# Optimization experiments

Measured on AMD Instinct MI355X. Metric: run time of the kernel, lower is better.

## Reference

```python
import jax, jax.numpy as jnp
import numpy as np

T = 2048          # tokens
H = 32            # query heads
HKV = 4           # kv heads
D = 128           # head dim
HID = 2048        # hidden size
EPS = 1e-6
THETA = 10000.0


def _rmsnorm(x, w):
    # x: [..., D]
    var = jnp.mean(x * x, axis=-1, keepdims=True)
    return x * jax.lax.rsqrt(var + EPS) * w


def _rope(x, positions):
    # neox-style rotary: x [T, h, D], positions [T]
    half = D // 2
    inv_freq = 1.0 / (THETA ** (jnp.arange(half, dtype=jnp.float32) * 2.0 / D))
    freqs = positions.astype(jnp.float32)[:, None] * inv_freq        # [T, D/2]
    cos = jnp.cos(freqs)[:, None, :]                                  # [T, 1, D/2]
    sin = jnp.sin(freqs)[:, None, :]
    x1, x2 = x[..., :half], x[..., half:]
    return jnp.concatenate([x1 * cos - x2 * sin, x2 * cos + x1 * sin], axis=-1)


def setup_inputs() -> dict:
    key = jax.random.key(0)
    k1, k2, k3 = jax.random.split(key, 3)
    scale_in = 1.0 / np.sqrt(HID)
    scale_o = 1.0 / np.sqrt(H * D)
    return {
        "hidden_states": jax.random.normal(k1, (T, HID), dtype=jnp.float32),
        "positions": jnp.arange(T, dtype=jnp.int32),
        "w_qkv": jax.random.normal(k2, (HID, (H + 2 * HKV) * D), dtype=jnp.float32) * scale_in,
        "w_o": jax.random.normal(k3, (H * D, HID), dtype=jnp.float32) * scale_o,
        "q_norm_w": jnp.ones((D,), dtype=jnp.float32),
        "k_norm_w": jnp.ones((D,), dtype=jnp.float32),
    }


def reference(hidden_states, positions, w_qkv, w_o, q_norm_w, k_norm_w):
    q_size, kv_size = H * D, HKV * D
    qkv = hidden_states @ w_qkv                                       # [T, (H+2*HKV)*D]
    q = qkv[:, :q_size].reshape(T, H, D)
    k = qkv[:, q_size:q_size + kv_size].reshape(T, HKV, D)
    v = qkv[:, q_size + kv_size:].reshape(T, HKV, D)

    # per-head RMSNorm on q/k, then RoPE
    q = _rope(_rmsnorm(q, q_norm_w), positions)
    k = _rope(_rmsnorm(k, k_norm_w), positions)

    # GQA: expand kv heads to query heads
    rep = H // HKV
    k = jnp.repeat(k, rep, axis=1)                                    # [T, H, D]
    v = jnp.repeat(v, rep, axis=1)

    scaling = D ** -0.5
    scores = jnp.einsum('qhd,khd->hqk', q, k) * scaling               # [H, T, T]
    causal = jnp.tril(jnp.ones((T, T), dtype=bool))
    scores = jnp.where(causal[None], scores, jnp.finfo(scores.dtype).min)
    probs = jax.nn.softmax(scores, axis=-1)
    attn = jnp.einsum('hqk,khd->qhd', probs, v).reshape(T, H * D)
    return attn @ w_o                                                 # [T, HID]
```

## Files before the change

kernel.cpp:

```cpp
#include <hip/hip_runtime.h>
#include <hip/hip_bf16.h>

typedef __attribute__((ext_vector_type(8))) __bf16 bf16x8;
typedef __attribute__((ext_vector_type(4))) __bf16 bf16x4;
typedef __attribute__((ext_vector_type(4))) float f32x4;
typedef __attribute__((ext_vector_type(16))) float f32x16;

#define T_TOK 2048
#define NH 32
#define NKV 4
#define HD 128
#define HID 2048
#define QKV_N 5120
#define QSZ 4096
#define KOFF 4096
#define VOFF 4608
#define ATT_N 4096

#define GLOAD_LDS16(g, l)                                              \
  __builtin_amdgcn_global_load_lds(                                    \
      (const __attribute__((address_space(1))) void*)(g),              \
      (__attribute__((address_space(3))) void*)(l), 16, 0, 0)

__global__ __launch_bounds__(256) void cast_f32_bf16(const float* __restrict__ in,
                                                     __bf16* __restrict__ out, int n4) {
  int i = blockIdx.x * 256 + threadIdx.x;
  if (i < n4) {
    float4 v = reinterpret_cast<const float4*>(in)[i];
    bf16x4 o;
    o[0] = (__bf16)v.x; o[1] = (__bf16)v.y; o[2] = (__bf16)v.z; o[3] = (__bf16)v.w;
    reinterpret_cast<bf16x4*>(out)[i] = o;
  }
}

__global__ __launch_bounds__(256) void transpose_cast(const float* __restrict__ in,
                                                      __bf16* __restrict__ out,
                                                      int R, int C) {
  __shared__ __attribute__((aligned(16))) __bf16 tile[64][72];
  const int c0 = blockIdx.x * 64;
  const int r0 = blockIdx.y * 64;
  const int ca = (threadIdx.x & 15) * 4;
  const int ra = (threadIdx.x >> 4) * 4;
  float4 v[4];
#pragma unroll
  for (int i = 0; i < 4; ++i)
    v[i] = *reinterpret_cast<const float4*>(&in[(size_t)(r0 + ra + i) * C + c0 + ca]);
#pragma unroll
  for (int j = 0; j < 4; ++j) {
    bf16x4 o;
#pragma unroll
    for (int i = 0; i < 4; ++i) o[i] = (__bf16)(((const float*)&v[i])[j]);
    *reinterpret_cast<bf16x4*>(&tile[ca + j][ra]) = o;
  }
  __syncthreads();
#pragma unroll
  for (int i = 0; i < 2; ++i) {
    int c = i * 32 + (threadIdx.x >> 3);
    int r8 = (threadIdx.x & 7) * 8;
    bf16x8 o = *reinterpret_cast<const bf16x8*>(&tile[c][r8]);
    *reinterpret_cast<bf16x8*>(&out[(size_t)(c0 + c) * R + r0 + r8]) = o;
  }
}

__global__ __launch_bounds__(256) void v_transpose(const __bf16* __restrict__ qkv,
                                                   __bf16* __restrict__ vt) {
  __shared__ __bf16 tile[64][72];
  int t0 = blockIdx.x * 64;
  int d0 = blockIdx.y * 64;
  int kvh = blockIdx.z;
  int tx = threadIdx.x & 63;
  int ty = threadIdx.x >> 6;
#pragma unroll
  for (int i = 0; i < 64; i += 4)
    tile[ty + i][tx] = qkv[(size_t)(t0 + ty + i) * QKV_N + VOFF + kvh * HD + d0 + tx];
  __syncthreads();
#pragma unroll
  for (int i = 0; i < 64; i += 4)
    vt[((size_t)kvh * HD + d0 + ty + i) * T_TOK + t0 + tx] = tile[tx][ty + i];
}

template <int OUTF32>
__global__ __launch_bounds__(256) void gemm_v9(const __bf16* __restrict__ A,
                                               const __bf16* __restrict__ B,
                                               void* __restrict__ Cp,
                                               int M, int N, int Ktot, int KS,
                                               int nby, int nks) {
  __shared__ __attribute__((aligned(16))) __bf16 As[3][128][32];
  __shared__ __attribute__((aligned(16))) __bf16 Bs[3][128][32];
  const int tid = threadIdx.x;
  const int lane = tid & 63;
  const int wave = tid >> 6;
  const int la = lane & 15;
  const int lb = lane >> 4;
  const int wr = (wave >> 1) * 64;
  const int wc = (wave & 1) * 64;

  const int nwg = gridDim.x;
  const int cpx = nwg >> 3;
  const int swz = ((int)blockIdx.x & 7) * cpx + ((int)blockIdx.x >> 3);
  const int ks = swz % nks;
  const int t2 = swz / nks;
  const int by = t2 % nby;
  const int bx = t2 / nby;
  const int rowA0 = by * 128;
  const int rowB0 = bx * 128;
  const int k00 = ks * KS;

  const int srow = wave * 16 + (lane >> 2);
  const int scol = (((lane & 3) * 16) ^ (((lane >> 2) & 3) << 4)) >> 1;
  const __bf16* Asrc0 = &A[(size_t)(rowA0 + srow) * Ktot + k00 + scol];
  const __bf16* Asrc1 = &A[(size_t)(rowA0 + 64 + srow) * Ktot + k00 + scol];
  const __bf16* Bsrc0 = &B[(size_t)(rowB0 + srow) * Ktot + k00 + scol];
  const __bf16* Bsrc1 = &B[(size_t)(rowB0 + 64 + srow) * Ktot + k00 + scol];

#define STAGEG(b, k0)                                            \
  do {                                                           \
    GLOAD_LDS16(Asrc0 + (k0), &As[b][wave * 16][0]);             \
    GLOAD_LDS16(Asrc1 + (k0), &As[b][64 + wave * 16][0]);        \
    GLOAD_LDS16(Bsrc0 + (k0), &Bs[b][wave * 16][0]);             \
    GLOAD_LDS16(Bsrc1 + (k0), &Bs[b][64 + wave * 16][0]);        \
  } while (0)

  f32x4 acc[4][4] = {};

  const int nt = KS >> 5;
  STAGEG(0, 0);
  STAGEG(1, 32);
  asm volatile("s_waitcnt vmcnt(4)" ::: "memory");
  __builtin_amdgcn_s_barrier();
  __builtin_amdgcn_sched_barrier(0);

  const int rdswz = (lb * 16) ^ ((la & 3) << 4);

  int cur = 0, stg = 2;
  for (int t = 0; t < nt; ++t) {
    if (t + 2 < nt) {
      STAGEG(stg, (t + 2) * 32);
    }

    const char* Ab = (const char*)&As[cur][0][0];
    const char* Bb = (const char*)&Bs[cur][0][0];
    bf16x8 af[4], bfr[4];
#pragma unroll
    for (int m = 0; m < 4; ++m)
      af[m] = *reinterpret_cast<const bf16x8*>(Ab + (wr + m * 16 + la) * 64 + rdswz);
#pragma unroll
    for (int n = 0; n < 4; ++n)
      bfr[n] = *reinterpret_cast<const bf16x8*>(Bb + (wc + n * 16 + la) * 64 + rdswz);
    __builtin_amdgcn_s_setprio(1);
#pragma unroll
    for (int m = 0; m < 4; ++m)
#pragma unroll
      for (int n = 0; n < 4; ++n)
        acc[m][n] = __builtin_amdgcn_mfma_f32_16x16x32_bf16(af[m], bfr[n], acc[m][n], 0, 0, 0);
    __builtin_amdgcn_s_setprio(0);

    const int rem = nt - 1 - t;
    if (rem >= 2) {
      asm volatile("s_waitcnt vmcnt(4)" ::: "memory");
    } else if (rem == 1) {
      asm volatile("s_waitcnt vmcnt(0)" ::: "memory");
    }
    if (rem) {
      __builtin_amdgcn_sched_barrier(0);
      __builtin_amdgcn_s_barrier();
      __builtin_amdgcn_sched_barrier(0);
    }
    cur = (cur == 2) ? 0 : cur + 1;
    stg = (stg == 2) ? 0 : stg + 1;
  }
#undef STAGEG

#pragma unroll
  for (int m = 0; m < 4; ++m) {
#pragma unroll
    for (int n = 0; n < 4; ++n) {
#pragma unroll
      for (int r = 0; r < 4; ++r) {
        int row = rowA0 + wr + m * 16 + lb * 4 + r;
        int col = rowB0 + wc + n * 16 + la;
        if (OUTF32) {
          float* pp = (float*)Cp + (size_t)ks * M * N;
          pp[(size_t)row * N + col] = acc[m][n][r];
        } else {
          reinterpret_cast<__bf16*>(Cp)[(size_t)row * N + col] = (__bf16)acc[m][n][r];
        }
      }
    }
  }
}

__global__ __launch_bounds__(256) void reduce2_f32(const float* __restrict__ pp,
                                                   float* __restrict__ out, int n4) {
  int i = blockIdx.x * 256 + threadIdx.x;
  if (i < n4) {
    float4 a = reinterpret_cast<const float4*>(pp)[i];
    float4 b = reinterpret_cast<const float4*>(pp + (size_t)HID * T_TOK)[i];
    float4 o;
    o.x = a.x + b.x; o.y = a.y + b.y; o.z = a.z + b.z; o.w = a.w + b.w;
    reinterpret_cast<float4*>(out)[i] = o;
  }
}

__global__ __launch_bounds__(64) void rope_table(const int* __restrict__ positions,
                                                 float* __restrict__ tab) {
  const int t = blockIdx.x;
  const int d = threadIdx.x;
  float freq = exp2f(-(float)d * 0.20762050593046015f);
  float fr = (float)positions[t] * freq;
  float c, s;
  sincosf(fr, &s, &c);
  tab[t * 128 + d] = c;
  tab[t * 128 + 64 + d] = s;
}

__global__ __launch_bounds__(128) void norm_rope(__bf16* __restrict__ qkv,
                                                 const float* __restrict__ tab,
                                                 const float* __restrict__ qw,
                                                 const float* __restrict__ kw) {
  const int t = blockIdx.x;
  const int head = blockIdx.y;
  const bool is_q = head < NH;
  const int col = is_q ? head * HD : KOFF + (head - NH) * HD;
  __bf16* row = qkv + (size_t)t * QKV_N + col;
  const int d = threadIdx.x;
  float x = (float)row[d];
  float ss = x * x;
#pragma unroll
  for (int mm = 1; mm < 64; mm <<= 1) ss += __shfl_xor(ss, mm);
  __shared__ float red[2];
  __shared__ float yl[128];
  if ((d & 63) == 0) red[d >> 6] = ss;
  __syncthreads();
  float var = (red[0] + red[1]) * (1.0f / 128.0f);
  float sc = rsqrtf(var + 1e-6f);
  const float* wv = is_q ? qw : kw;
  yl[d] = x * sc * wv[d];
  __syncthreads();
  if (d < 64) {
    float x1 = yl[d], x2 = yl[d + 64];
    float c = tab[t * 128 + d];
    float sn = tab[t * 128 + 64 + d];
    row[d] = (__bf16)(x1 * c - x2 * sn);
    row[d + 64] = (__bf16)(x2 * c + x1 * sn);
  }
}

__device__ __forceinline__ uint32_t pkbf(float a, float b) {
  union { __bf16 h; unsigned short u; } x, y;
  x.h = (__bf16)a;
  y.h = (__bf16)b;
  return (uint32_t)x.u | ((uint32_t)y.u << 16);
}

__global__ __launch_bounds__(256, 2) void flash_attn5(const __bf16* __restrict__ qkv,
                                                      const __bf16* __restrict__ vt,
                                                      __bf16* __restrict__ attn) {
  __shared__ __attribute__((aligned(16))) __bf16 lds[32768];

  const int tid = threadIdx.x;
  const int lane = tid & 63;
  const int wave = tid >> 6;
  const int q5 = lane & 31;
  const int hi = lane >> 5;
  const int yy = blockIdx.x;
  const int kvh = yy >> 1;
  const int h = kvh * 8 + (yy & 1) * 4 + wave;
  const __bf16* Kbase = qkv + KOFF + kvh * HD;
  const __bf16* Vbase = vt + (size_t)kvh * HD * T_TOK;

  const int qt = 63 - (int)blockIdx.y;
  const int qb = qt * 32;
  const int qrow = qb + q5;
  const int nt = (qb + 32 + 63) >> 6;

  const float qscale = 0.088388347648318447f * 1.4426950408889634f;

  bf16x8 qf[8];
  {
    const __bf16* Qp = qkv + (size_t)(qb + q5) * QKV_N + h * HD + hi * 8;
#pragma unroll
    for (int k0 = 0; k0 < 8; ++k0) {
      bf16x8 q = *reinterpret_cast<const bf16x8*>(Qp + k0 * 16);
#pragma unroll
      for (int j = 0; j < 8; ++j) q[j] = (__bf16)((float)q[j] * qscale);
      qf[k0] = q;
    }
  }

  const int kc = (lane & 15) * 16;
  const int vc = (lane & 7) * 16;

#define STAGE5(b, kv00)                                                         \
  do {                                                                          \
    __bf16* kdst = lds + (b) * 8192;                                            \
    __bf16* vdst = lds + 16384 + (b) * 8192;                                    \
    _Pragma("unroll")                                                           \
    for (int i = 0; i < 4; ++i) {                                               \
      int kr = wave * 16 + i * 4 + (lane >> 4);                                 \
      int ksc = (kc ^ ((kr & 15) << 4)) >> 1;                                   \
      GLOAD_LDS16(Kbase + (size_t)((kv00) + kr) * QKV_N + ksc,                  \
                  kdst + (wave * 16 + i * 4) * 128);                            \
      int vr = wave * 32 + i * 8 + (lane >> 3);                                 \
      int vsc = (vc ^ ((vr & 7) << 4)) >> 1;                                    \
      GLOAD_LDS16(Vbase + (size_t)vr * T_TOK + (kv00) + vsc,                    \
                  vdst + (wave * 32 + i * 8) * 64);                             \
    }                                                                           \
  } while (0)

  f32x16 acc0 = {}, acc1 = {}, acc2 = {}, acc3 = {};
  float mrow = -1e30f, lrow = 0.0f;

  STAGE5(0, 0);

  int cur = 0;
  for (int t = 0; t < nt; ++t) {
    const int kv0 = t * 64;
    __builtin_amdgcn_s_barrier();
    __builtin_amdgcn_sched_barrier(0);
    if (t + 1 < nt) {
      STAGE5(cur ^ 1, kv0 + 64);
      asm volatile("s_waitcnt vmcnt(8)" ::: "memory");
    } else {
      asm volatile("s_waitcnt vmcnt(0)" ::: "memory");
    }
    __builtin_amdgcn_s_barrier();
    __builtin_amdgcn_sched_barrier(0);

    const char* Kt = (const char*)(lds + cur * 8192);
    const char* Vt = (const char*)(lds + 16384 + cur * 8192);

    f32x16 st0 = {}, st1 = {};
    __builtin_amdgcn_s_setprio(1);
#pragma unroll
    for (int k0 = 0; k0 < 8; ++k0) {
      int cS = (k0 * 32 + hi * 16) ^ ((q5 & 15) << 4);
      bf16x8 a0 = *reinterpret_cast<const bf16x8*>(Kt + q5 * 256 + cS);
      bf16x8 a1 = *reinterpret_cast<const bf16x8*>(Kt + (32 + q5) * 256 + cS);
      st0 = __builtin_amdgcn_mfma_f32_32x32x16_bf16(a0, qf[k0], st0, 0, 0, 0);
      st1 = __builtin_amdgcn_mfma_f32_32x32x16_bf16(a1, qf[k0], st1, 0, 0, 0);
    }
    __builtin_amdgcn_s_setprio(0);

    if (!(kv0 + 63 <= qb)) {
#pragma unroll
      for (int r = 0; r < 16; ++r) {
        int kp = kv0 + (r & 3) + 8 * (r >> 2) + 4 * hi;
        if (kp > qrow) st0[r] = -1e30f;
        if (kp + 32 > qrow) st1[r] = -1e30f;
      }
    }
    float mx = -1e30f;
#pragma unroll
    for (int r = 0; r < 16; ++r) mx = fmaxf(mx, fmaxf(st0[r], st1[r]));
    mx = fmaxf(mx, __shfl_xor(mx, 32));
    if (__any(mx > mrow + 8.0f)) {
      float mnew = fmaxf(mrow, mx);
      float corr = exp2f(mrow - mnew);
      lrow *= corr;
      acc0 *= corr; acc1 *= corr; acc2 *= corr; acc3 *= corr;
      mrow = mnew;
    }
    float ps = 0.0f;
#pragma unroll
    for (int r = 0; r < 16; ++r) {
      float p0 = exp2f(st0[r] - mrow);
      float p1 = exp2f(st1[r] - mrow);
      ps += p0 + p1;
      st0[r] = p0;
      st1[r] = p1;
    }
    ps += __shfl_xor(ps, 32);
    lrow += ps;

    uint32_t W0[8], W1[8];
#pragma unroll
    for (int m = 0; m < 8; ++m) {
      W0[m] = pkbf(st0[2 * m], st0[2 * m + 1]);
      W1[m] = pkbf(st1[2 * m], st1[2 * m + 1]);
    }

    const bool hib = (hi != 0);
#pragma unroll
    for (int ks = 0; ks < 4; ++ks) {
      const int j = 4 * (ks & 1);
      uint32_t wj0, wj1, wj2, wj3;
      if (ks < 2) { wj0 = W0[j]; wj1 = W0[j + 1]; wj2 = W0[j + 2]; wj3 = W0[j + 3]; }
      else        { wj0 = W1[j]; wj1 = W1[j + 1]; wj2 = W1[j + 2]; wj3 = W1[j + 3]; }
      uint32_t keepA = hib ? wj2 : wj0;
      uint32_t keepB = hib ? wj3 : wj1;
      uint32_t sendA = hib ? wj0 : wj2;
      uint32_t sendB = hib ? wj1 : wj3;
      uint32_t recvA = (uint32_t)__shfl_xor((int)sendA, 32);
      uint32_t recvB = (uint32_t)__shfl_xor((int)sendB, 32);
      union { uint32_t u[4]; bf16x8 v; } fr;
      fr.u[0] = hib ? recvA : keepA;
      fr.u[1] = hib ? recvB : keepB;
      fr.u[2] = hib ? keepA : recvA;
      fr.u[3] = hib ? keepB : recvB;
      const int cV = (ks * 32 + hi * 16) ^ ((q5 & 7) << 4);
      __builtin_amdgcn_s_setprio(1);
      bf16x8 v0 = *reinterpret_cast<const bf16x8*>(Vt + (0 * 32 + q5) * 128 + cV);
      acc0 = __builtin_amdgcn_mfma_f32_32x32x16_bf16(v0, fr.v, acc0, 0, 0, 0);
      bf16x8 v1 = *reinterpret_cast<const bf16x8*>(Vt + (1 * 32 + q5) * 128 + cV);
      acc1 = __builtin_amdgcn_mfma_f32_32x32x16_bf16(v1, fr.v, acc1, 0, 0, 0);
      bf16x8 v2 = *reinterpret_cast<const bf16x8*>(Vt + (2 * 32 + q5) * 128 + cV);
      acc2 = __builtin_amdgcn_mfma_f32_32x32x16_bf16(v2, fr.v, acc2, 0, 0, 0);
      bf16x8 v3 = *reinterpret_cast<const bf16x8*>(Vt + (3 * 32 + q5) * 128 + cV);
      acc3 = __builtin_amdgcn_mfma_f32_32x32x16_bf16(v3, fr.v, acc3, 0, 0, 0);
      __builtin_amdgcn_s_setprio(0);
    }
    cur ^= 1;
  }

  __syncthreads();
  {
    char* ob = (char*)lds + wave * 8192;
    float inv = 1.0f / lrow;
    const int swzE = (q5 & 15) << 4;
#pragma unroll
    for (int dt = 0; dt < 4; ++dt) {
      f32x16 a = dt == 0 ? acc0 : dt == 1 ? acc1 : dt == 2 ? acc2 : acc3;
#pragma unroll
      for (int t4 = 0; t4 < 4; ++t4) {
        uint2 wv;
        wv.x = pkbf(a[4 * t4] * inv, a[4 * t4 + 1] * inv);
        wv.y = pkbf(a[4 * t4 + 2] * inv, a[4 * t4 + 3] * inv);
        int d2 = (dt * 32 + 8 * t4 + 4 * hi) * 2;
        *reinterpret_cast<uint2*>(ob + q5 * 256 + (d2 ^ swzE)) = wv;
      }
    }
#pragma unroll
    for (int rr = 0; rr < 8; ++rr) {
      int idx = rr * 64 + lane;
      int q = idx >> 4;
      int cc = (idx & 15) * 16;
      bf16x8 o = *reinterpret_cast<const bf16x8*>(ob + q * 256 + (cc ^ ((q & 15) << 4)));
      *reinterpret_cast<bf16x8*>(&attn[(size_t)(qb + q) * ATT_N + h * HD + (cc >> 1)]) = o;
    }
  }
}

extern "C" void kernel_launch(void* const* d_in, const int* in_sizes, int n_in,
                              void* d_out, int out_size, void* d_ws, size_t ws_size,
                              hipStream_t stream) {
  const float* hs   = (const float*)d_in[0];
  const int*   pos  = (const int*)d_in[1];
  const float* wqkv = (const float*)d_in[2];
  const float* wo   = (const float*)d_in[3];
  const float* qw   = (const float*)d_in[4];
  const float* kw   = (const float*)d_in[5];
  float* out = (float*)d_out;

  char* p = (char*)d_ws;
  __bf16* hsb   = (__bf16*)p; p += (size_t)T_TOK * HID * 2;
  __bf16* wqkvT = (__bf16*)p; p += (size_t)QKV_N * HID * 2;
  __bf16* woT   = (__bf16*)p; p += (size_t)HID * QSZ * 2;
  __bf16* qkvb  = (__bf16*)p; p += (size_t)T_TOK * QKV_N * 2;
  __bf16* attnb = (__bf16*)p; p += (size_t)T_TOK * QSZ * 2;
  __bf16* vtb   = (__bf16*)p; p += (size_t)NKV * HD * T_TOK * 2;
  float*  ropet = (float*)p;  p += (size_t)T_TOK * HD * 4;
  float*  oprt  = (float*)p;  p += (size_t)2 * T_TOK * HID * 4;

  cast_f32_bf16<<<(T_TOK * HID / 4) / 256, 256, 0, stream>>>(hs, hsb, T_TOK * HID / 4);
  transpose_cast<<<dim3(QKV_N / 64, HID / 64), 256, 0, stream>>>(wqkv, wqkvT, HID, QKV_N);
  transpose_cast<<<dim3(HID / 64, QSZ / 64), 256, 0, stream>>>(wo, woT, QSZ, HID);
  rope_table<<<T_TOK, 64, 0, stream>>>(pos, ropet);
  gemm_v9<0><<<(QKV_N / 128) * (T_TOK / 128), 256, 0, stream>>>(
      hsb, wqkvT, qkvb, T_TOK, QKV_N, HID, HID, T_TOK / 128, 1);
  norm_rope<<<dim3(T_TOK, NH + NKV), 128, 0, stream>>>(qkvb, ropet, qw, kw);
  v_transpose<<<dim3(T_TOK / 64, HD / 64, NKV), 256, 0, stream>>>(qkvb, vtb);
  flash_attn5<<<dim3(8, 64), 256, 0, stream>>>(qkvb, vtb, attnb);
  gemm_v9<1><<<2 * (HID / 128) * (T_TOK / 128), 256, 0, stream>>>(
      attnb, woT, oprt, T_TOK, HID, QSZ, QSZ / 2, T_TOK / 128, 2);
  reduce2_f32<<<(T_TOK * HID / 4 + 255) / 256, 256, 0, stream>>>(
      oprt, out, T_TOK * HID / 4);
}
```

Measured before the change: 250.3 us.

## Split attention KV range across two wave groups with in-block softmax merge

The flash attention kernel now launches 512 threads per block. Two groups of four waves each process half of the KV tiles for the same query tile, using 32-key tiles instead of 64. At the end, the second group writes its partial outputs (stored as bf16) and its row max and sum to LDS, and the first group merges them with rescaling before the store. This aims to raise occupancy and parallelism and shorten the serial KV loop, at the cost of 64KB of LDS per block, extra barriers, a merge pass, and bf16 rounding of the partial accumulators.

```diff
diff --git a/kernel.cpp b/kernel.cpp
--- a/kernel.cpp
+++ b/kernel.cpp
@@ -253,26 +253,32 @@
   return (uint32_t)x.u | ((uint32_t)y.u << 16);
 }
 
-__global__ __launch_bounds__(256, 2) void flash_attn5(const __bf16* __restrict__ qkv,
+__global__ __launch_bounds__(512, 4) void flash_attn6(const __bf16* __restrict__ qkv,
                                                       const __bf16* __restrict__ vt,
                                                       __bf16* __restrict__ attn) {
-  __shared__ __attribute__((aligned(16))) __bf16 lds[32768];
+  __shared__ __attribute__((aligned(16))) char ldsB[65536];
 
   const int tid = threadIdx.x;
   const int lane = tid & 63;
   const int wave = tid >> 6;
+  const int half = wave >> 2;
+  const int wh = wave & 3;
   const int q5 = lane & 31;
   const int hi = lane >> 5;
-  const int yy = blockIdx.x;
-  const int kvh = yy >> 1;
-  const int h = kvh * 8 + (yy & 1) * 4 + wave;
+  const int xx = blockIdx.x;
+  const int kvh = xx >> 1;
+  const int h = kvh * 8 + (xx & 1) * 4 + wh;
   const __bf16* Kbase = qkv + KOFF + kvh * HD;
   const __bf16* Vbase = vt + (size_t)kvh * HD * T_TOK;
 
   const int qt = 63 - (int)blockIdx.y;
   const int qb = qt * 32;
   const int qrow = qb + q5;
-  const int nt = (qb + 32 + 63) >> 6;
+  const int nt = qt + 1;
+  const int mid = nt >> 1;
+  const int iters = nt - mid;
+  const int tbase = half ? mid : 0;
+  const int mycnt = half ? iters : mid;
 
   const float qscale = 0.088388347648318447f * 1.4426950408889634f;
 
@@ -288,144 +294,176 @@
     }
   }
 
-  const int kc = (lane & 15) * 16;
-  const int vc = (lane & 7) * 16;
-
-#define STAGE5(b, kv00)                                                         \
-  do {                                                                          \
-    __bf16* kdst = lds + (b) * 8192;                                            \
-    __bf16* vdst = lds + 16384 + (b) * 8192;                                    \
-    _Pragma("unroll")                                                           \
-    for (int i = 0; i < 4; ++i) {                                               \
-      int kr = wave * 16 + i * 4 + (lane >> 4);                                 \
-      int ksc = (kc ^ ((kr & 15) << 4)) >> 1;                                   \
-      GLOAD_LDS16(Kbase + (size_t)((kv00) + kr) * QKV_N + ksc,                  \
-                  kdst + (wave * 16 + i * 4) * 128);                            \
-      int vr = wave * 32 + i * 8 + (lane >> 3);                                 \
-      int vsc = (vc ^ ((vr & 7) << 4)) >> 1;                                    \
-      GLOAD_LDS16(Vbase + (size_t)vr * T_TOK + (kv00) + vsc,                    \
-                  vdst + (wave * 32 + i * 8) * 64);                             \
-    }                                                                           \
+  const int ku0 = wh * 2, ku1 = wh * 2 + 1;
+  const int krow0 = ku0 * 4 + (lane >> 4);
+  const int krow1 = ku1 * 4 + (lane >> 4);
+  const int kcB = (lane & 15) * 16;
+  const int ksc0 = (kcB ^ ((krow0 & 15) << 4)) >> 1;
+  const int ksc1 = (kcB ^ ((krow1 & 15) << 4)) >> 1;
+  const int vrow0 = ku0 * 16 + (lane >> 2);
+  const int vrow1 = ku1 * 16 + (lane >> 2);
+  const int vcB = (lane & 3) * 16;
+  const int vsc0 = (vcB ^ ((vrow0 & 3) << 4)) >> 1;
+  const int vsc1 = (vcB ^ ((vrow1 & 3) << 4)) >> 1;
+
+#define STAGE6(b, kv00)                                                        \
+  do {                                                                         \
+    char* base = ldsB + ((b) * 2 + half) * 16384;                              \
+    GLOAD_LDS16(Kbase + (size_t)((kv00) + krow0) * QKV_N + ksc0,               \
+                base + ku0 * 1024);                                            \
+    GLOAD_LDS16(Kbase + (size_t)((kv00) + krow1) * QKV_N + ksc1,               \
+                base + ku1 * 1024);                                            \
+    GLOAD_LDS16(Vbase + (size_t)vrow0 * T_TOK + (kv00) + vsc0,                 \
+                base + 8192 + ku0 * 1024);                                     \
+    GLOAD_LDS16(Vbase + (size_t)vrow1 * T_TOK + (kv00) + vsc1,                 \
+                base + 8192 + ku1 * 1024);                                     \
   } while (0)
 
   f32x16 acc0 = {}, acc1 = {}, acc2 = {}, acc3 = {};
   float mrow = -1e30f, lrow = 0.0f;
 
-  STAGE5(0, 0);
+  if (mycnt > 0) STAGE6(0, tbase * 32);
 
   int cur = 0;
-  for (int t = 0; t < nt; ++t) {
-    const int kv0 = t * 64;
+  for (int t = 0; t < iters; ++t) {
     __builtin_amdgcn_s_barrier();
     __builtin_amdgcn_sched_barrier(0);
-    if (t + 1 < nt) {
-      STAGE5(cur ^ 1, kv0 + 64);
-      asm volatile("s_waitcnt vmcnt(8)" ::: "memory");
+    if (t + 1 < mycnt) {
+      STAGE6(cur ^ 1, (tbase + t + 1) * 32);
+      asm volatile("s_waitcnt vmcnt(4)" ::: "memory");
     } else {
       asm volatile("s_waitcnt vmcnt(0)" ::: "memory");
     }
     __builtin_amdgcn_s_barrier();
     __builtin_amdgcn_sched_barrier(0);
 
-    const char* Kt = (const char*)(lds + cur * 8192);
-    const char* Vt = (const char*)(lds + 16384 + cur * 8192);
-
-    f32x16 st0 = {}, st1 = {};
-    __builtin_amdgcn_s_setprio(1);
-#pragma unroll
-    for (int k0 = 0; k0 < 8; ++k0) {
-      int cS = (k0 * 32 + hi * 16) ^ ((q5 & 15) << 4);
-      bf16x8 a0 = *reinterpret_cast<const bf16x8*>(Kt + q5 * 256 + cS);
-      bf16x8 a1 = *reinterpret_cast<const bf16x8*>(Kt + (32 + q5) * 256 + cS);
-      st0 = __builtin_amdgcn_mfma_f32_32x32x16_bf16(a0, qf[k0], st0, 0, 0, 0);
-      st1 = __builtin_amdgcn_mfma_f32_32x32x16_bf16(a1, qf[k0], st1, 0, 0, 0);
-    }
-    __builtin_amdgcn_s_setprio(0);
-
-    if (!(kv0 + 63 <= qb)) {
+    if (t < mycnt) {
+      const int kv0 = (tbase + t) * 32;
+      const char* Kt = ldsB + (cur * 2 + half) * 16384;
+      const char* Vt = Kt + 8192;
+
+      f32x16 st = {};
+      __builtin_amdgcn_s_setprio(1);
+#pragma unroll
+      for (int k0 = 0; k0 < 8; ++k0) {
+        int cS = (k0 * 32 + hi * 16) ^ ((q5 & 15) << 4);
+        bf16x8 a0 = *reinterpret_cast<const bf16x8*>(Kt + q5 * 256 + cS);
+        st = __builtin_amdgcn_mfma_f32_32x32x16_bf16(a0, qf[k0], st, 0, 0, 0);
+      }
+      __builtin_amdgcn_s_setprio(0);
+
+      if (kv0 + 31 > qb) {
+#pragma unroll
+        for (int r = 0; r < 16; ++r) {
+          int kp = kv0 + (r & 3) + 8 * (r >> 2) + 4 * hi;
+          if (kp > qrow) st[r] = -1e30f;
+        }
+      }
+      float mx = -1e30f;
+#pragma unroll
+      for (int r = 0; r < 16; ++r) mx = fmaxf(mx, st[r]);
+      mx = fmaxf(mx, __shfl_xor(mx, 32));
+      if (__any(mx > mrow + 8.0f)) {
+        float mnew = fmaxf(mrow, mx);
+        float corr = exp2f(mrow - mnew);
+        lrow *= corr;
+        acc0 *= corr; acc1 *= corr; acc2 *= corr; acc3 *= corr;
+        mrow = mnew;
+      }
+      float ps = 0.0f;
 #pragma unroll
       for (int r = 0; r < 16; ++r) {
-        int kp = kv0 + (r & 3) + 8 * (r >> 2) + 4 * hi;
-        if (kp > qrow) st0[r] = -1e30f;
-        if (kp + 32 > qrow) st1[r] = -1e30f;
-      }
-    }
-    float mx = -1e30f;
-#pragma unroll
-    for (int r = 0; r < 16; ++r) mx = fmaxf(mx, fmaxf(st0[r], st1[r]));
-    mx = fmaxf(mx, __shfl_xor(mx, 32));
-    if (__any(mx > mrow + 8.0f)) {
-      float mnew = fmaxf(mrow, mx);
-      float corr = exp2f(mrow - mnew);
-      lrow *= corr;
-      acc0 *= corr; acc1 *= corr; acc2 *= corr; acc3 *= corr;
-      mrow = mnew;
-    }
-    float ps = 0.0f;
-#pragma unroll
-    for (int r = 0; r < 16; ++r) {
-      float p0 = exp2f(st0[r] - mrow);
-      float p1 = exp2f(st1[r] - mrow);
-      ps += p0 + p1;
-      st0[r] = p0;
-      st1[r] = p1;
-    }
-    ps += __shfl_xor(ps, 32);
-    lrow += ps;
-
-    uint32_t W0[8], W1[8];
-#pragma unroll
-    for (int m = 0; m < 8; ++m) {
-      W0[m] = pkbf(st0[2 * m], st0[2 * m + 1]);
-      W1[m] = pkbf(st1[2 * m], st1[2 * m + 1]);
-    }
-
-    const bool hib = (hi != 0);
-#pragma unroll
-    for (int ks = 0; ks < 4; ++ks) {
-      const int j = 4 * (ks & 1);
-      uint32_t wj0, wj1, wj2, wj3;
-      if (ks < 2) { wj0 = W0[j]; wj1 = W0[j + 1]; wj2 = W0[j + 2]; wj3 = W0[j + 3]; }
-      else        { wj0 = W1[j]; wj1 = W1[j + 1]; wj2 = W1[j + 2]; wj3 = W1[j + 3]; }
-      uint32_t keepA = hib ? wj2 : wj0;
-      uint32_t keepB = hib ? wj3 : wj1;
-      uint32_t sendA = hib ? wj0 : wj2;
-      uint32_t sendB = hib ? wj1 : wj3;
-      uint32_t recvA = (uint32_t)__shfl_xor((int)sendA, 32);
-      uint32_t recvB = (uint32_t)__shfl_xor((int)sendB, 32);
-      union { uint32_t u[4]; bf16x8 v; } fr;
-      fr.u[0] = hib ? recvA : keepA;
-      fr.u[1] = hib ? recvB : keepB;
-      fr.u[2] = hib ? keepA : recvA;
-      fr.u[3] = hib ? keepB : recvB;
-      const int cV = (ks * 32 + hi * 16) ^ ((q5 & 7) << 4);
-      __builtin_amdgcn_s_setprio(1);
-      bf16x8 v0 = *reinterpret_cast<const bf16x8*>(Vt + (0 * 32 + q5) * 128 + cV);
-      acc0 = __builtin_amdgcn_mfma_f32_32x32x16_bf16(v0, fr.v, acc0, 0, 0, 0);
-      bf16x8 v1 = *reinterpret_cast<const bf16x8*>(Vt + (1 * 32 + q5) * 128 + cV);
-      acc1 = __builtin_amdgcn_mfma_f32_32x32x16_bf16(v1, fr.v, acc1, 0, 0, 0);
-      bf16x8 v2 = *reinterpret_cast<const bf16x8*>(Vt + (2 * 32 + q5) * 128 + cV);
-      acc2 = __builtin_amdgcn_mfma_f32_32x32x16_bf16(v2, fr.v, acc2, 0, 0, 0);
-      bf16x8 v3 = *reinterpret_cast<const bf16x8*>(Vt + (3 * 32 + q5) * 128 + cV);
-      acc3 = __builtin_amdgcn_mfma_f32_32x32x16_bf16(v3, fr.v, acc3, 0, 0, 0);
-      __builtin_amdgcn_s_setprio(0);
+        float p = exp2f(st[r] - mrow);
+        ps += p;
+        st[r] = p;
+      }
+      ps += __shfl_xor(ps, 32);
+      lrow += ps;
+
+      uint32_t W[8];
+#pragma unroll
+      for (int m = 0; m < 8; ++m) W[m] = pkbf(st[2 * m], st[2 * m + 1]);
+
+      const bool hib = (hi != 0);
+#pragma unroll
+      for (int ks = 0; ks < 2; ++ks) {
+        const int j = 4 * ks;
+        uint32_t keepA = hib ? W[j + 2] : W[j];
+        uint32_t keepB = hib ? W[j + 3] : W[j + 1];
+        uint32_t sendA = hib ? W[j] : W[j + 2];
+        uint32_t sendB = hib ? W[j + 1] : W[j + 3];
+        uint32_t recvA = (uint32_t)__shfl_xor((int)sendA, 32);
+        uint32_t recvB = (uint32_t)__shfl_xor((int)sendB, 32);
+        union { uint32_t u[4]; bf16x8 v; } fr;
+        fr.u[0] = hib ? recvA : keepA;
+        fr.u[1] = hib ? recvB : keepB;
+        fr.u[2] = hib ? keepA : recvA;
+        fr.u[3] = hib ? keepB : recvB;
+        __builtin_amdgcn_s_setprio(1);
+#pragma unroll
+        for (int dt = 0; dt < 4; ++dt) {
+          const int row = dt * 32 + q5;
+          bf16x8 v = *reinterpret_cast<const bf16x8*>(
+              Vt + row * 64 + ((ks * 32 + hi * 16) ^ ((row & 3) << 4)));
+          if (dt == 0) acc0 = __builtin_amdgcn_mfma_f32_32x32x16_bf16(v, fr.v, acc0, 0, 0, 0);
+          else if (dt == 1) acc1 = __builtin_amdgcn_mfma_f32_32x32x16_bf16(v, fr.v, acc1, 0, 0, 0);
+          else if (dt == 2) acc2 = __builtin_amdgcn_mfma_f32_32x32x16_bf16(v, fr.v, acc2, 0, 0, 0);
+          else acc3 = __builtin_amdgcn_mfma_f32_32x32x16_bf16(v, fr.v, acc3, 0, 0, 0);
+        }
+        __builtin_amdgcn_s_setprio(0);
+      }
     }
     cur ^= 1;
   }
-
-  __syncthreads();
-  {
-    char* ob = (char*)lds + wave * 8192;
-    float inv = 1.0f / lrow;
-    const int swzE = (q5 & 15) << 4;
+#undef STAGE6
+
+  __syncthreads();
+  __bf16* Osh = (__bf16*)(ldsB + wh * 8192);
+  float2* mlsh = (float2*)(ldsB + 32768);
+  if (half == 1) {
 #pragma unroll
     for (int dt = 0; dt < 4; ++dt) {
       f32x16 a = dt == 0 ? acc0 : dt == 1 ? acc1 : dt == 2 ? acc2 : acc3;
 #pragma unroll
+      for (int r = 0; r < 16; ++r) {
+        int row = dt * 32 + (r & 3) + 8 * (r >> 2) + 4 * hi;
+        Osh[row * 32 + q5] = (__bf16)a[r];
+      }
+    }
+    if (hi == 0) mlsh[wh * 32 + q5] = make_float2(mrow, lrow);
+  }
+  __syncthreads();
+  if (half == 0) {
+    float2 ml1 = mlsh[wh * 32 + q5];
+    float m = fmaxf(mrow, ml1.x);
+    float c0 = exp2f(mrow - m);
+    float c1 = exp2f(ml1.x - m);
+    float inv = 1.0f / (lrow * c0 + ml1.y * c1);
+#pragma unroll
+    for (int dt = 0; dt < 4; ++dt) {
+      f32x16 a = dt == 0 ? acc0 : dt == 1 ? acc1 : dt == 2 ? acc2 : acc3;
+#pragma unroll
+      for (int r = 0; r < 16; ++r) {
+        int row = dt * 32 + (r & 3) + 8 * (r >> 2) + 4 * hi;
+        a[r] = (a[r] * c0 + (float)Osh[row * 32 + q5] * c1) * inv;
+      }
+      if (dt == 0) acc0 = a; else if (dt == 1) acc1 = a;
+      else if (dt == 2) acc2 = a; else acc3 = a;
+    }
+  }
+  __syncthreads();
+
+  if (half == 0) {
+    char* ob = ldsB + wh * 8192;
+    const int swzE = (q5 & 15) << 4;
+#pragma unroll
+    for (int dt = 0; dt < 4; ++dt) {
+      f32x16 a = dt == 0 ? acc0 : dt == 1 ? acc1 : dt == 2 ? acc2 : acc3;
+#pragma unroll
       for (int t4 = 0; t4 < 4; ++t4) {
         uint2 wv;
-        wv.x = pkbf(a[4 * t4] * inv, a[4 * t4 + 1] * inv);
-        wv.y = pkbf(a[4 * t4 + 2] * inv, a[4 * t4 + 3] * inv);
+        wv.x = pkbf(a[4 * t4], a[4 * t4 + 1]);
+        wv.y = pkbf(a[4 * t4 + 2], a[4 * t4 + 3]);
         int d2 = (dt * 32 + 8 * t4 + 4 * hi) * 2;
         *reinterpret_cast<uint2*>(ob + q5 * 256 + (d2 ^ swzE)) = wv;
       }
@@ -470,7 +508,7 @@
       hsb, wqkvT, qkvb, T_TOK, QKV_N, HID, HID, T_TOK / 128, 1);
   norm_rope<<<dim3(T_TOK, NH + NKV), 128, 0, stream>>>(qkvb, ropet, qw, kw);
   v_transpose<<<dim3(T_TOK / 64, HD / 64, NKV), 256, 0, stream>>>(qkvb, vtb);
-  flash_attn5<<<dim3(8, 64), 256, 0, stream>>>(qkvb, vtb, attnb);
+  flash_attn6<<<dim3(8, 64), 512, 0, stream>>>(qkvb, vtb, attnb);
   gemm_v9<1><<<2 * (HID / 128) * (T_TOK / 128), 256, 0, stream>>>(
       attnb, woT, oprt, T_TOK, HID, QSZ, QSZ / 2, T_TOK / 128, 2);
   reduce2_f32<<<(T_TOK * HID / 4 + 255) / 256, 256, 0, stream>>>(
```

New measurement: 318.1 us. 27.1% more time.

## Process two query heads per wave to reuse staged K/V tiles

Applied to the files above, without the earlier changes.

Each flash-attention block now covers all 8 query heads of a KV head: every wave computes two heads against the same LDS-resident K/V tiles, halving the grid to 4x64 blocks. This halves the K/V global-to-LDS traffic and the LDS fragment reads per unit of MFMA work. In exchange, register pressure roughly doubles (launch bounds drop to 1 block per CU), and with only 256 blocks the GPU may be underfilled, so latency hiding suffers.

```diff
diff --git a/kernel.cpp b/kernel.cpp
--- a/kernel.cpp
+++ b/kernel.cpp
@@ -253,7 +253,7 @@
   return (uint32_t)x.u | ((uint32_t)y.u << 16);
 }
 
-__global__ __launch_bounds__(256, 2) void flash_attn5(const __bf16* __restrict__ qkv,
+__global__ __launch_bounds__(256, 1) void flash_attn7(const __bf16* __restrict__ qkv,
                                                       const __bf16* __restrict__ vt,
                                                       __bf16* __restrict__ attn) {
   __shared__ __attribute__((aligned(16))) __bf16 lds[32768];
@@ -263,9 +263,9 @@
   const int wave = tid >> 6;
   const int q5 = lane & 31;
   const int hi = lane >> 5;
-  const int yy = blockIdx.x;
-  const int kvh = yy >> 1;
-  const int h = kvh * 8 + (yy & 1) * 4 + wave;
+  const int kvh = blockIdx.x;
+  const int hA = kvh * 8 + wave;
+  const int hB = kvh * 8 + 4 + wave;
   const __bf16* Kbase = qkv + KOFF + kvh * HD;
   const __bf16* Vbase = vt + (size_t)kvh * HD * T_TOK;
 
@@ -276,22 +276,28 @@
 
   const float qscale = 0.088388347648318447f * 1.4426950408889634f;
 
-  bf16x8 qf[8];
+  bf16x8 qfA[8], qfB[8];
   {
-    const __bf16* Qp = qkv + (size_t)(qb + q5) * QKV_N + h * HD + hi * 8;
+    const __bf16* QpA = qkv + (size_t)(qb + q5) * QKV_N + hA * HD + hi * 8;
+    const __bf16* QpB = qkv + (size_t)(qb + q5) * QKV_N + hB * HD + hi * 8;
 #pragma unroll
     for (int k0 = 0; k0 < 8; ++k0) {
-      bf16x8 q = *reinterpret_cast<const bf16x8*>(Qp + k0 * 16);
-#pragma unroll
-      for (int j = 0; j < 8; ++j) q[j] = (__bf16)((float)q[j] * qscale);
-      qf[k0] = q;
+      bf16x8 qa = *reinterpret_cast<const bf16x8*>(QpA + k0 * 16);
+      bf16x8 qb8 = *reinterpret_cast<const bf16x8*>(QpB + k0 * 16);
+#pragma unroll
+      for (int j = 0; j < 8; ++j) {
+        qa[j] = (__bf16)((float)qa[j] * qscale);
+        qb8[j] = (__bf16)((float)qb8[j] * qscale);
+      }
+      qfA[k0] = qa;
+      qfB[k0] = qb8;
     }
   }
 
   const int kc = (lane & 15) * 16;
   const int vc = (lane & 7) * 16;
 
-#define STAGE5(b, kv00)                                                         \
+#define STAGE7(b, kv00)                                                         \
   do {                                                                          \
     __bf16* kdst = lds + (b) * 8192;                                            \
     __bf16* vdst = lds + 16384 + (b) * 8192;                                    \
@@ -308,10 +314,12 @@
     }                                                                           \
   } while (0)
 
-  f32x16 acc0 = {}, acc1 = {}, acc2 = {}, acc3 = {};
-  float mrow = -1e30f, lrow = 0.0f;
-
-  STAGE5(0, 0);
+  f32x16 accA0 = {}, accA1 = {}, accA2 = {}, accA3 = {};
+  f32x16 accB0 = {}, accB1 = {}, accB2 = {}, accB3 = {};
+  float mrowA = -1e30f, lrowA = 0.0f;
+  float mrowB = -1e30f, lrowB = 0.0f;
+
+  STAGE7(0, 0);
 
   int cur = 0;
   for (int t = 0; t < nt; ++t) {
@@ -319,7 +327,7 @@
     __builtin_amdgcn_s_barrier();
     __builtin_amdgcn_sched_barrier(0);
     if (t + 1 < nt) {
-      STAGE5(cur ^ 1, kv0 + 64);
+      STAGE7(cur ^ 1, kv0 + 64);
       asm volatile("s_waitcnt vmcnt(8)" ::: "memory");
     } else {
       asm volatile("s_waitcnt vmcnt(0)" ::: "memory");
@@ -330,15 +338,17 @@
     const char* Kt = (const char*)(lds + cur * 8192);
     const char* Vt = (const char*)(lds + 16384 + cur * 8192);
 
-    f32x16 st0 = {}, st1 = {};
+    f32x16 sA0 = {}, sA1 = {}, sB0 = {}, sB1 = {};
     __builtin_amdgcn_s_setprio(1);
 #pragma unroll
     for (int k0 = 0; k0 < 8; ++k0) {
       int cS = (k0 * 32 + hi * 16) ^ ((q5 & 15) << 4);
       bf16x8 a0 = *reinterpret_cast<const bf16x8*>(Kt + q5 * 256 + cS);
       bf16x8 a1 = *reinterpret_cast<const bf16x8*>(Kt + (32 + q5) * 256 + cS);
-      st0 = __builtin_amdgcn_mfma_f32_32x32x16_bf16(a0, qf[k0], st0, 0, 0, 0);
-      st1 = __builtin_amdgcn_mfma_f32_32x32x16_bf16(a1, qf[k0], st1, 0, 0, 0);
+      sA0 = __builtin_amdgcn_mfma_f32_32x32x16_bf16(a0, qfA[k0], sA0, 0, 0, 0);
+      sB0 = __builtin_amdgcn_mfma_f32_32x32x16_bf16(a0, qfB[k0], sB0, 0, 0, 0);
+      sA1 = __builtin_amdgcn_mfma_f32_32x32x16_bf16(a1, qfA[k0], sA1, 0, 0, 0);
+      sB1 = __builtin_amdgcn_mfma_f32_32x32x16_bf16(a1, qfB[k0], sB1, 0, 0, 0);
     }
     __builtin_amdgcn_s_setprio(0);
 
@@ -346,97 +356,147 @@
 #pragma unroll
       for (int r = 0; r < 16; ++r) {
         int kp = kv0 + (r & 3) + 8 * (r >> 2) + 4 * hi;
-        if (kp > qrow) st0[r] = -1e30f;
-        if (kp + 32 > qrow) st1[r] = -1e30f;
-      }
-    }
-    float mx = -1e30f;
-#pragma unroll
-    for (int r = 0; r < 16; ++r) mx = fmaxf(mx, fmaxf(st0[r], st1[r]));
-    mx = fmaxf(mx, __shfl_xor(mx, 32));
-    if (__any(mx > mrow + 8.0f)) {
-      float mnew = fmaxf(mrow, mx);
-      float corr = exp2f(mrow - mnew);
-      lrow *= corr;
-      acc0 *= corr; acc1 *= corr; acc2 *= corr; acc3 *= corr;
-      mrow = mnew;
-    }
-    float ps = 0.0f;
+        if (kp > qrow) { sA0[r] = -1e30f; sB0[r] = -1e30f; }
+        if (kp + 32 > qrow) { sA1[r] = -1e30f; sB1[r] = -1e30f; }
+      }
+    }
+
+    float mxA = -1e30f, mxB = -1e30f;
 #pragma unroll
     for (int r = 0; r < 16; ++r) {
-      float p0 = exp2f(st0[r] - mrow);
-      float p1 = exp2f(st1[r] - mrow);
-      ps += p0 + p1;
-      st0[r] = p0;
-      st1[r] = p1;
-    }
-    ps += __shfl_xor(ps, 32);
-    lrow += ps;
-
-    uint32_t W0[8], W1[8];
+      mxA = fmaxf(mxA, fmaxf(sA0[r], sA1[r]));
+      mxB = fmaxf(mxB, fmaxf(sB0[r], sB1[r]));
+    }
+    mxA = fmaxf(mxA, __shfl_xor(mxA, 32));
+    mxB = fmaxf(mxB, __shfl_xor(mxB, 32));
+    if (__any(mxA > mrowA + 8.0f)) {
+      float mnew = fmaxf(mrowA, mxA);
+      float corr = exp2f(mrowA - mnew);
+      lrowA *= corr;
+      accA0 *= corr; accA1 *= corr; accA2 *= corr; accA3 *= corr;
+      mrowA = mnew;
+    }
+    if (__any(mxB > mrowB + 8.0f)) {
+      float mnew = fmaxf(mrowB, mxB);
+      float corr = exp2f(mrowB - mnew);
+      lrowB *= corr;
+      accB0 *= corr; accB1 *= corr; accB2 *= corr; accB3 *= corr;
+      mrowB = mnew;
+    }
+    float psA = 0.0f, psB = 0.0f;
+#pragma unroll
+    for (int r = 0; r < 16; ++r) {
+      float pa0 = exp2f(sA0[r] - mrowA);
+      float pa1 = exp2f(sA1[r] - mrowA);
+      float pb0 = exp2f(sB0[r] - mrowB);
+      float pb1 = exp2f(sB1[r] - mrowB);
+      psA += pa0 + pa1;
+      psB += pb0 + pb1;
+      sA0[r] = pa0; sA1[r] = pa1; sB0[r] = pb0; sB1[r] = pb1;
+    }
+    psA += __shfl_xor(psA, 32);
+    psB += __shfl_xor(psB, 32);
+    lrowA += psA;
+    lrowB += psB;
+
+    uint32_t WA0[8], WA1[8], WB0[8], WB1[8];
 #pragma unroll
     for (int m = 0; m < 8; ++m) {
-      W0[m] = pkbf(st0[2 * m], st0[2 * m + 1]);
-      W1[m] = pkbf(st1[2 * m], st1[2 * m + 1]);
+      WA0[m] = pkbf(sA0[2 * m], sA0[2 * m + 1]);
+      WA1[m] = pkbf(sA1[2 * m], sA1[2 * m + 1]);
+      WB0[m] = pkbf(sB0[2 * m], sB0[2 * m + 1]);
+      WB1[m] = pkbf(sB1[2 * m], sB1[2 * m + 1]);
     }
 
     const bool hib = (hi != 0);
 #pragma unroll
     for (int ks = 0; ks < 4; ++ks) {
       const int j = 4 * (ks & 1);
-      uint32_t wj0, wj1, wj2, wj3;
-      if (ks < 2) { wj0 = W0[j]; wj1 = W0[j + 1]; wj2 = W0[j + 2]; wj3 = W0[j + 3]; }
-      else        { wj0 = W1[j]; wj1 = W1[j + 1]; wj2 = W1[j + 2]; wj3 = W1[j + 3]; }
-      uint32_t keepA = hib ? wj2 : wj0;
-      uint32_t keepB = hib ? wj3 : wj1;
-      uint32_t sendA = hib ? wj0 : wj2;
-      uint32_t sendB = hib ? wj1 : wj3;
-      uint32_t recvA = (uint32_t)__shfl_xor((int)sendA, 32);
-      uint32_t recvB = (uint32_t)__shfl_xor((int)sendB, 32);
-      union { uint32_t u[4]; bf16x8 v; } fr;
-      fr.u[0] = hib ? recvA : keepA;
-      fr.u[1] = hib ? recvB : keepB;
-      fr.u[2] = hib ? keepA : recvA;
-      fr.u[3] = hib ? keepB : recvB;
+      uint32_t a0, a1, a2, a3, b0, b1, b2, b3;
+      if (ks < 2) {
+        a0 = WA0[j]; a1 = WA0[j + 1]; a2 = WA0[j + 2]; a3 = WA0[j + 3];
+        b0 = WB0[j]; b1 = WB0[j + 1]; b2 = WB0[j + 2]; b3 = WB0[j + 3];
+      } else {
+        a0 = WA1[j]; a1 = WA1[j + 1]; a2 = WA1[j + 2]; a3 = WA1[j + 3];
+        b0 = WB1[j]; b1 = WB1[j + 1]; b2 = WB1[j + 2]; b3 = WB1[j + 3];
+      }
+      union { uint32_t u[4]; bf16x8 v; } frA, frB;
+      {
+        uint32_t keepA = hib ? a2 : a0, keepB = hib ? a3 : a1;
+        uint32_t sendA = hib ? a0 : a2, sendB = hib ? a1 : a3;
+        uint32_t recvA = (uint32_t)__shfl_xor((int)sendA, 32);
+        uint32_t recvB = (uint32_t)__shfl_xor((int)sendB, 32);
+        frA.u[0] = hib ? recvA : keepA;
+        frA.u[1] = hib ? recvB : keepB;
+        frA.u[2] = hib ? keepA : recvA;
+        frA.u[3] = hib ? keepB : recvB;
+      }
+      {
+        uint32_t keepA = hib ? b2 : b0, keepB = hib ? b3 : b1;
+        uint32_t sendA = hib ? b0 : b2, sendB = hib ? b1 : b3;
+        uint32_t recvA = (uint32_t)__shfl_xor((int)sendA, 32);
+        uint32_t recvB = (uint32_t)__shfl_xor((int)sendB, 32);
+        frB.u[0] = hib ? recvA : keepA;
+        frB.u[1] = hib ? recvB : keepB;
+        frB.u[2] = hib ? keepA : recvA;
+        frB.u[3] = hib ? keepB : recvB;
+      }
       const int cV = (ks * 32 + hi * 16) ^ ((q5 & 7) << 4);
       __builtin_amdgcn_s_setprio(1);
-      bf16x8 v0 = *reinterpret_cast<const bf16x8*>(Vt + (0 * 32 + q5) * 128 + cV);
-      acc0 = __builtin_amdgcn_mfma_f32_32x32x16_bf16(v0, fr.v, acc0, 0, 0, 0);
-      bf16x8 v1 = *reinterpret_cast<const bf16x8*>(Vt + (1 * 32 + q5) * 128 + cV);
-      acc1 = __builtin_amdgcn_mfma_f32_32x32x16_bf16(v1, fr.v, acc1, 0, 0, 0);
-      bf16x8 v2 = *reinterpret_cast<const bf16x8*>(Vt + (2 * 32 + q5) * 128 + cV);
-      acc2 = __builtin_amdgcn_mfma_f32_32x32x16_bf16(v2, fr.v, acc2, 0, 0, 0);
-      bf16x8 v3 = *reinterpret_cast<const bf16x8*>(Vt + (3 * 32 + q5) * 128 + cV);
-      acc3 = __builtin_amdgcn_mfma_f32_32x32x16_bf16(v3, fr.v, acc3, 0, 0, 0);
+      {
+        bf16x8 v0 = *reinterpret_cast<const bf16x8*>(Vt + (0 * 32 + q5) * 128 + cV);
+        accA0 = __builtin_amdgcn_mfma_f32_32x32x16_bf16(v0, frA.v, accA0, 0, 0, 0);
+        accB0 = __builtin_amdgcn_mfma_f32_32x32x16_bf16(v0, frB.v, accB0, 0, 0, 0);
+        bf16x8 v1 = *reinterpret_cast<const bf16x8*>(Vt + (1 * 32 + q5) * 128 + cV);
+        accA1 = __builtin_amdgcn_mfma_f32_32x32x16_bf16(v1, frA.v, accA1, 0, 0, 0);
+        accB1 = __builtin_amdgcn_mfma_f32_32x32x16_bf16(v1, frB.v, accB1, 0, 0, 0);
+        bf16x8 v2 = *reinterpret_cast<const bf16x8*>(Vt + (2 * 32 + q5) * 128 + cV);
+        accA2 = __builtin_amdgcn_mfma_f32_32x32x16_bf16(v2, frA.v, accA2, 0, 0, 0);
+        accB2 = __builtin_amdgcn_mfma_f32_32x32x16_bf16(v2, frB.v, accB2, 0, 0, 0);
+        bf16x8 v3 = *reinterpret_cast<const bf16x8*>(Vt + (3 * 32 + q5) * 128 + cV);
+        accA3 = __builtin_amdgcn_mfma_f32_32x32x16_bf16(v3, frA.v, accA3, 0, 0, 0);
+        accB3 = __builtin_amdgcn_mfma_f32_32x32x16_bf16(v3, frB.v, accB3, 0, 0, 0);
+      }
       __builtin_amdgcn_s_setprio(0);
     }
     cur ^= 1;
   }
+#undef STAGE7
 
   __syncthreads();
   {
     char* ob = (char*)lds + wave * 8192;
-    float inv = 1.0f / lrow;
     const int swzE = (q5 & 15) << 4;
-#pragma unroll
-    for (int dt = 0; dt < 4; ++dt) {
-      f32x16 a = dt == 0 ? acc0 : dt == 1 ? acc1 : dt == 2 ? acc2 : acc3;
-#pragma unroll
-      for (int t4 = 0; t4 < 4; ++t4) {
-        uint2 wv;
-        wv.x = pkbf(a[4 * t4] * inv, a[4 * t4 + 1] * inv);
-        wv.y = pkbf(a[4 * t4 + 2] * inv, a[4 * t4 + 3] * inv);
-        int d2 = (dt * 32 + 8 * t4 + 4 * hi) * 2;
-        *reinterpret_cast<uint2*>(ob + q5 * 256 + (d2 ^ swzE)) = wv;
-      }
-    }
-#pragma unroll
-    for (int rr = 0; rr < 8; ++rr) {
-      int idx = rr * 64 + lane;
-      int q = idx >> 4;
-      int cc = (idx & 15) * 16;
-      bf16x8 o = *reinterpret_cast<const bf16x8*>(ob + q * 256 + (cc ^ ((q & 15) << 4)));
-      *reinterpret_cast<bf16x8*>(&attn[(size_t)(qb + q) * ATT_N + h * HD + (cc >> 1)]) = o;
+    const float invA = 1.0f / lrowA;
+    const float invB = 1.0f / lrowB;
+#pragma unroll
+    for (int hsel = 0; hsel < 2; ++hsel) {
+      const float inv = hsel ? invB : invA;
+      const int h = hsel ? hB : hA;
+#pragma unroll
+      for (int dt = 0; dt < 4; ++dt) {
+        f32x16 a;
+        if (hsel == 0)
+          a = dt == 0 ? accA0 : dt == 1 ? accA1 : dt == 2 ? accA2 : accA3;
+        else
+          a = dt == 0 ? accB0 : dt == 1 ? accB1 : dt == 2 ? accB2 : accB3;
+#pragma unroll
+        for (int t4 = 0; t4 < 4; ++t4) {
+          uint2 wv;
+          wv.x = pkbf(a[4 * t4] * inv, a[4 * t4 + 1] * inv);
+          wv.y = pkbf(a[4 * t4 + 2] * inv, a[4 * t4 + 3] * inv);
+          int d2 = (dt * 32 + 8 * t4 + 4 * hi) * 2;
+          *reinterpret_cast<uint2*>(ob + q5 * 256 + (d2 ^ swzE)) = wv;
+        }
+      }
+#pragma unroll
+      for (int rr = 0; rr < 8; ++rr) {
+        int idx = rr * 64 + lane;
+        int q = idx >> 4;
+        int cc = (idx & 15) * 16;
+        bf16x8 o = *reinterpret_cast<const bf16x8*>(ob + q * 256 + (cc ^ ((q & 15) << 4)));
+        *reinterpret_cast<bf16x8*>(&attn[(size_t)(qb + q) * ATT_N + h * HD + (cc >> 1)]) = o;
+      }
     }
   }
 }
@@ -470,7 +530,7 @@
       hsb, wqkvT, qkvb, T_TOK, QKV_N, HID, HID, T_TOK / 128, 1);
   norm_rope<<<dim3(T_TOK, NH + NKV), 128, 0, stream>>>(qkvb, ropet, qw, kw);
   v_transpose<<<dim3(T_TOK / 64, HD / 64, NKV), 256, 0, stream>>>(qkvb, vtb);
-  flash_attn5<<<dim3(8, 64), 256, 0, stream>>>(qkvb, vtb, attnb);
+  flash_attn7<<<dim3(NKV, 64), 256, 0, stream>>>(qkvb, vtb, attnb);
   gemm_v9<1><<<2 * (HID / 128) * (T_TOK / 128), 256, 0, stream>>>(
       attnb, woT, oprt, T_TOK, HID, QSZ, QSZ / 2, T_TOK / 128, 2);
   reduce2_f32<<<(T_TOK * HID / 4 + 255) / 256, 256, 0, stream>>>(
```

After: 302.9 us. 1.21x slower.
